# Performance work log

Hardware: AMD Instinct MI355X
Metric: run time of the kernel (lower is better)

Reference implementation:

```python
import jax, jax.numpy as jnp
import numpy as np

EPS_MSG = 1e-7
EPS_BN = 1e-5


def _seg_softmax(logits, seg, num_segments):
    # logits: [E, D] per-edge logits; softmax over edges sharing the same dst node
    m = jax.ops.segment_max(logits, seg, num_segments=num_segments)
    m = jnp.where(jnp.isfinite(m), m, 0.0)
    e = jnp.exp(logits - m[seg])
    s = jax.ops.segment_sum(e, seg, num_segments=num_segments)
    return e / (s[seg] + 1e-16)


def _batchnorm(h, gamma, beta):
    mu = jnp.mean(h, axis=0)
    var = jnp.var(h, axis=0)
    return (h - mu) * jax.lax.rsqrt(var + EPS_BN) * gamma + beta


def setup_inputs() -> dict:
    key = jax.random.key(0)
    ks = jax.random.split(key, 12)
    N, E, G, D, L = 100000, 600000, 512, 128, 7
    x = jax.random.randint(ks[0], (N, 9), 0, 64, dtype=jnp.int32)
    edge_index = jax.random.randint(ks[1], (2, E), 0, N, dtype=jnp.int32)
    edge_attr = jax.random.randint(ks[2], (E, 3), 0, 8, dtype=jnp.int32)
    batch = jnp.sort(jax.random.randint(ks[3], (N,), 0, G, dtype=jnp.int32))
    rf_pred = jax.random.uniform(ks[4], (G,), dtype=jnp.float32)
    atom_emb = jax.random.normal(ks[5], (9, 64, D), dtype=jnp.float32) * 0.02
    bond_emb = jax.random.normal(ks[6], (3, 8, D), dtype=jnp.float32) * 0.02
    conv_w = jax.random.normal(ks[7], (L, D, D), dtype=jnp.float32) * 0.02
    conv_b = jnp.zeros((L, D), dtype=jnp.float32)
    ts = jnp.ones((L,), dtype=jnp.float32)  # learnable inverse temperatures (init 1/t style)
    gammas = jnp.ones((L, D), dtype=jnp.float32)
    bn_betas = jnp.zeros((L, D), dtype=jnp.float32)
    final_w = jax.random.normal(ks[8], (D, 1), dtype=jnp.float32) * 0.02
    final_b = jnp.zeros((1,), dtype=jnp.float32)
    beta = jnp.array([0.5], dtype=jnp.float32)
    return {"x": x, "edge_index": edge_index, "edge_attr": edge_attr, "batch": batch,
            "rf_pred": rf_pred, "atom_emb": atom_emb, "bond_emb": bond_emb,
            "conv_w": conv_w, "conv_b": conv_b, "ts": ts, "gammas": gammas,
            "bn_betas": bn_betas, "final_w": final_w, "final_b": final_b, "beta": beta}


def reference(x, edge_index, edge_attr, batch, rf_pred, atom_emb, bond_emb,
              conv_w, conv_b, ts, gammas, bn_betas, final_w, final_b, beta):
    N = x.shape[0]
    G = rf_pred.shape[0]
    L = conv_w.shape[0]
    src, dst = edge_index[0], edge_index[1]

    # AtomEncoder / BondEncoder: sum of per-feature embeddings
    h = jax.vmap(lambda tab, idx: tab[idx], in_axes=(0, 1))(atom_emb, x).sum(0)          # [N, D]
    e_emb = jax.vmap(lambda tab, idx: tab[idx], in_axes=(0, 1))(bond_emb, edge_attr).sum(0)  # [E, D]

    def genconv(l, hin):
        msg = jax.nn.relu(hin[src] + e_emb) + EPS_MSG          # [E, D]
        alpha = _seg_softmax(msg * ts[l], dst, N)              # softmax aggregation weights
        aggr = jax.ops.segment_sum(alpha * msg, dst, num_segments=N)  # [N, D]
        return (hin + aggr) @ conv_w[l] + conv_b[l]

    # res+ DeeperGCN
    h = genconv(0, h)
    for l in range(1, L):
        h2 = jax.nn.relu(_batchnorm(h, gammas[l - 1], bn_betas[l - 1]))
        h = genconv(l, h2) + h
    h = jax.nn.relu(_batchnorm(h, gammas[L - 1], bn_betas[L - 1]))

    # mean graph pooling
    counts = jnp.maximum(jax.ops.segment_sum(jnp.ones((N,), h.dtype), batch, num_segments=G), 1.0)
    hg = jax.ops.segment_sum(h, batch, num_segments=G) / counts[:, None]  # [G, D]

    dgcn_pred = hg @ final_w + final_b  # [G, 1]
    return (1.0 - beta) * jax.nn.sigmoid(dgcn_pred) + beta * rf_pred.reshape(-1, 1)
```

## Files before the change

### kernel.cpp

```cpp
#include <hip/hip_runtime.h>
#include <hip/hip_fp16.h>
#include <math.h>

#define D 128
#define PF 12

typedef _Float16 f16x8 __attribute__((ext_vector_type(8)));
typedef float f32x4_t __attribute__((ext_vector_type(4)));


__global__ void hist_kernel(const int* __restrict__ edge_index, int* __restrict__ deg, int E) {
    int e = blockIdx.x * blockDim.x + threadIdx.x;
    if (e >= E) return;
    atomicAdd(&deg[edge_index[E + e]], 1);
}

__global__ void scanA_kernel(const int* __restrict__ deg, int* __restrict__ bsum, int n) {
    __shared__ int red[256];
    int b = blockIdx.x, t = threadIdx.x;
    int base = b * 1024 + t * 4;
    int s = 0;
#pragma unroll
    for (int j = 0; j < 4; ++j)
        if (base + j < n) s += deg[base + j];
    red[t] = s;
    __syncthreads();
    for (int off = 128; off > 0; off >>= 1) {
        if (t < off) red[t] += red[t + off];
        __syncthreads();
    }
    if (t == 0) bsum[b] = red[0];
}

__global__ void scanB_kernel(int* __restrict__ bsum, int nb) {
    __shared__ int sh[256];
    int t = threadIdx.x;
    sh[t] = (t < nb) ? bsum[t] : 0;
    __syncthreads();
    for (int off = 1; off < 256; off <<= 1) {
        int v = (t >= off) ? sh[t - off] : 0;
        __syncthreads();
        sh[t] += v;
        __syncthreads();
    }
    if (t < nb) bsum[t] = (t == 0) ? 0 : sh[t - 1];
}

__global__ void scanC_kernel(const int* __restrict__ deg, const int* __restrict__ boff,
                             int* __restrict__ row_start, int* __restrict__ cursor, int n) {
    __shared__ int sh[256];
    int b = blockIdx.x, t = threadIdx.x;
    int base = b * 1024 + t * 4;
    int v[4];
#pragma unroll
    for (int j = 0; j < 4; ++j) v[j] = (base + j < n) ? deg[base + j] : 0;
    int p[4];
    p[0] = 0; p[1] = v[0]; p[2] = v[0] + v[1]; p[3] = v[0] + v[1] + v[2];
    int s = p[3] + v[3];
    sh[t] = s;
    __syncthreads();
    for (int off = 1; off < 256; off <<= 1) {
        int x = (t >= off) ? sh[t - off] : 0;
        __syncthreads();
        sh[t] += x;
        __syncthreads();
    }
    int off0 = boff[b] + sh[t] - s;
#pragma unroll
    for (int j = 0; j < 4; ++j)
        if (base + j < n) {
            row_start[base + j] = off0 + p[j];
            cursor[base + j] = off0 + p[j];
        }
    if (base <= n - 1 && n - 1 < base + 4) row_start[n] = off0 + s;
}

__global__ void scatter_kernel(const int* __restrict__ edge_index, const int* __restrict__ edge_attr,
                               int* __restrict__ cursor, int2* __restrict__ csr, int E) {
    int e = blockIdx.x * blockDim.x + threadIdx.x;
    if (e >= E) return;
    int src = edge_index[e];
    int dst = edge_index[E + e];
    int pos = atomicAdd(&cursor[dst], 1);
    int a0 = edge_attr[e * 3], a1 = edge_attr[e * 3 + 1], a2 = edge_attr[e * 3 + 2];
    csr[pos] = make_int2(src, a0 | (a1 << 3) | (a2 << 6));
}

__global__ void misc_build_kernel(const float* __restrict__ bond_emb, __half2* __restrict__ evt,
                                  const float* __restrict__ conv_w, _Float16* __restrict__ wt,
                                  int wtTotal, const int* __restrict__ batch,
                                  int* __restrict__ gstart, int N, int G) {
    int idx = blockIdx.x * blockDim.x + threadIdx.x;
    if (idx < 512 * 64) {
        int combo = idx >> 6, j = idx & 63;
        int d0 = 2 * j;
        float ex = bond_emb[(combo & 7) * D + d0] +
                   bond_emb[(8 + ((combo >> 3) & 7)) * D + d0] +
                   bond_emb[(16 + ((combo >> 6) & 7)) * D + d0];
        float ey = bond_emb[(combo & 7) * D + d0 + 1] +
                   bond_emb[(8 + ((combo >> 3) & 7)) * D + d0 + 1] +
                   bond_emb[(16 + ((combo >> 6) & 7)) * D + d0 + 1];
        evt[idx] = __floats2half2_rn(ex, ey);
        return;
    }
    int widx = idx - 512 * 64;
    if (widx < wtTotal) {
        int l = widx >> 14;
        int rem = widx & 16383;
        int n = rem >> 7, k = rem & 127;
        wt[widx] = (_Float16)conv_w[(l << 14) + k * 128 + n];
        return;
    }
    int n = widx - wtTotal;
    if (n >= N) return;
    if (n == 0) {
        for (int g = 0; g <= batch[0]; ++g) gstart[g] = 0;
    } else {
        int b0 = batch[n - 1], b1 = batch[n];
        for (int g = b0 + 1; g <= b1; ++g) gstart[g] = n;
    }
    if (n == N - 1) {
        for (int g = batch[N - 1] + 1; g <= G; ++g) gstart[g] = N;
    }
}


__global__ void atom_embed_kernel(const int* __restrict__ x,
                                  const float* __restrict__ atom_emb,
                                  _Float16* __restrict__ h16, int N) {
    long long idx = (long long)blockIdx.x * blockDim.x + threadIdx.x;
    if (idx >= (long long)N * D) return;
    int n = (int)(idx >> 7);
    int d = (int)(idx & 127);
    float acc = 0.f;
#pragma unroll
    for (int f = 0; f < 9; ++f) {
        int v = x[n * 9 + f];
        acc += atom_emb[(long long)(f * 64 + v) * D + d];
    }
    h16[idx] = (_Float16)acc;
}

__global__ void bn_reduce_finalize_kernel(const float* __restrict__ partial, int nb,
                                          const float* __restrict__ gamma,
                                          const float* __restrict__ bnbeta, float invN,
                                          float* __restrict__ aArr, float* __restrict__ bArr) {
    __shared__ float r1[256], r2[256];
    int d = blockIdx.x, t = threadIdx.x;
    float a1 = 0.f, a2 = 0.f;
    for (int i = t; i < nb; i += 256) {
        a1 += partial[(long long)i * 256 + d];
        a2 += partial[(long long)i * 256 + 128 + d];
    }
    r1[t] = a1; r2[t] = a2;
    __syncthreads();
    for (int off = 128; off > 0; off >>= 1) {
        if (t < off) { r1[t] += r1[t + off]; r2[t] += r2[t + off]; }
        __syncthreads();
    }
    if (t == 0) {
        float mean = r1[0] * invN;
        float var = r2[0] * invN - mean * mean;
        float a = rsqrtf(var + 1e-5f) * gamma[d];
        aArr[d] = a;
        bArr[d] = bnbeta[d] - mean * a;
    }
}

__global__ __launch_bounds__(128, 8) void fused_layer_kernel(
        const __half2* __restrict__ h16c,
        const float* __restrict__ aArr, const float* __restrict__ bArr, int applyBN,
        const float* __restrict__ ts, int l,
        const int* __restrict__ row_start, const int2* __restrict__ csr,
        const __half2* __restrict__ evt,
        const _Float16* __restrict__ wt, const float* __restrict__ bias,
        int residual, _Float16* __restrict__ h16out,
        float* __restrict__ partial, int N) {
    __shared__ __align__(16) char smem[8192];
    _Float16* yh = (_Float16*)smem;
    __half2* tile = (__half2*)smem;

    int t = threadIdx.x;
    int row0 = blockIdx.x * 16;
    int wave = t >> 6;
    int lane = t & 63;
    float tsl = ts[l];
    int a = row0 + wave * 8;

    float2 bnA = make_float2(1.f, 0.f), bnB = make_float2(0.f, 0.f);
    if (applyBN) {
        bnA = ((const float2*)aArr)[lane];
        bnB = ((const float2*)bArr)[lane];
    }

    int rsv = row_start[min(a + min(lane, 8), N)];
    __half2 zero2 = __floats2half2_rn(0.f, 0.f);
    __half2 hsv0 = zero2, hsv1 = zero2, hsv2 = zero2, hsv3 = zero2;
    __half2 hsv4 = zero2, hsv5 = zero2, hsv6 = zero2, hsv7 = zero2;
    if (a + 0 < N) hsv0 = h16c[(size_t)(a + 0) * 64 + lane];
    if (a + 1 < N) hsv1 = h16c[(size_t)(a + 1) * 64 + lane];
    if (a + 2 < N) hsv2 = h16c[(size_t)(a + 2) * 64 + lane];
    if (a + 3 < N) hsv3 = h16c[(size_t)(a + 3) * 64 + lane];
    if (a + 4 < N) hsv4 = h16c[(size_t)(a + 4) * 64 + lane];
    if (a + 5 < N) hsv5 = h16c[(size_t)(a + 5) * 64 + lane];
    if (a + 6 < N) hsv6 = h16c[(size_t)(a + 6) * 64 + lane];
    if (a + 7 < N) hsv7 = h16c[(size_t)(a + 7) * 64 + lane];

    int s0 = __builtin_amdgcn_readlane(rsv, 0);
    int s1 = __builtin_amdgcn_readlane(rsv, 8);

    int c0 = s0;
    int2 eaCur = make_int2(0, 0), eaNxt = make_int2(0, 0);
    if (c0 + lane < s1) eaCur = csr[c0 + lane];
    if (c0 + 64 + lane < s1) eaNxt = csr[c0 + 64 + lane];

    __half2 hvS[PF], evS[PF];
#pragma unroll
    for (int k = 0; k < PF; ++k) {
        int pp = s0 + k;
        if (pp < s1) {
            int srcp = __builtin_amdgcn_readlane(eaCur.x, k);
            int cbp = __builtin_amdgcn_readlane(eaCur.y, k);
            hvS[k] = h16c[(size_t)srcp * 64 + lane];
            evS[k] = evt[(size_t)cbp * 64 + lane];
        }
    }

    float accwx = 0.f, accwy = 0.f, accmx = 0.f, accmy = 0.f;
    int cur = 0;
    int nend = __builtin_amdgcn_readlane(rsv, 1);

#define CLOSE_ROW()                                                          \
    {                                                                        \
        __half2 hh;                                                          \
        switch (cur) {                                                       \
            case 0: hh = hsv0; break;                                        \
            case 1: hh = hsv1; break;                                        \
            case 2: hh = hsv2; break;                                        \
            case 3: hh = hsv3; break;                                        \
            case 4: hh = hsv4; break;                                        \
            case 5: hh = hsv5; break;                                        \
            case 6: hh = hsv6; break;                                        \
            default: hh = hsv7; break;                                       \
        }                                                                    \
        float2 hs2 = __half22float2(hh);                                     \
        if (applyBN) {                                                       \
            hs2.x = fmaxf(hs2.x * bnA.x + bnB.x, 0.f);                       \
            hs2.y = fmaxf(hs2.y * bnA.y + bnB.y, 0.f);                       \
        }                                                                    \
        float2 yy;                                                           \
        yy.x = hs2.x + accmx / (accwx + 1e-16f);                             \
        yy.y = hs2.y + accmy / (accwy + 1e-16f);                             \
        tile[(wave * 8 + cur) * 68 + lane] = __floats2half2_rn(yy.x, yy.y);  \
        accwx = accwy = accmx = accmy = 0.f;                                 \
        cur++;                                                               \
        nend = __builtin_amdgcn_readlane(rsv, min(cur + 1, 8));              \
    }

    while (cur < 8 && nend == s0) CLOSE_ROW();

    int total = s1 - s0;
    for (int it = 0; it < total; it += PF) {
#pragma unroll
        for (int k = 0; k < PF; ++k) {
            int p = s0 + it + k;
            if (p < s1) {
                float2 hv = __half22float2(hvS[k]);
                float2 ev = __half22float2(evS[k]);
                if (applyBN) {
                    hv.x = fmaxf(hv.x * bnA.x + bnB.x, 0.f);
                    hv.y = fmaxf(hv.y * bnA.y + bnB.y, 0.f);
                }
                float mx = fmaxf(hv.x + ev.x, 0.f) + 1e-7f;
                float my = fmaxf(hv.y + ev.y, 0.f) + 1e-7f;
                float wx = __expf(mx * tsl);
                float wy = __expf(my * tsl);
                accwx += wx; accmx += wx * mx;
                accwy += wy; accmy += wy * my;
                int pp = p + PF;
                if (pp < s1) {
                    if (pp >= c0 + 64) {
                        c0 += 64;
                        eaCur = eaNxt;
                        eaNxt = make_int2(0, 0);
                        if (c0 + 64 + lane < s1) eaNxt = csr[c0 + 64 + lane];
                    }
                    int q = pp - c0;
                    int srcp = __builtin_amdgcn_readlane(eaCur.x, q);
                    int cbp = __builtin_amdgcn_readlane(eaCur.y, q);
                    hvS[k] = h16c[(size_t)srcp * 64 + lane];
                    evS[k] = evt[(size_t)cbp * 64 + lane];
                }
                while (cur < 8 && nend == p + 1) CLOSE_ROW();
            }
        }
    }
#undef CLOSE_ROW
    __syncthreads();

    int ln = t & 15;
    int quad = (t & 63) >> 4;
    const _Float16* h16in = (const _Float16*)h16c;

    float cs[4] = {0.f, 0.f, 0.f, 0.f};
    float cq[4] = {0.f, 0.f, 0.f, 0.f};
    const _Float16* ap = yh + ln * 136 + quad * 8;
#pragma unroll
    for (int ct = 0; ct < 4; ++ct) {
        int colg = (wave * 4 + ct) * 16 + ln;
        const _Float16* bp = wt + (size_t)colg * 128 + quad * 8;
        f32x4_t c = {0.f, 0.f, 0.f, 0.f};
#pragma unroll
        for (int kk = 0; kk < 4; ++kk) {
            f16x8 av = *(const f16x8*)(ap + kk * 32);
            f16x8 bv = *(const f16x8*)(bp + kk * 32);
            c = __builtin_amdgcn_mfma_f32_16x16x32_f16(av, bv, c, 0, 0, 0);
        }
        float bsv = bias[colg];
#pragma unroll
        for (int reg = 0; reg < 4; ++reg) {
            int r = row0 + quad * 4 + reg;
            if (r < N) {
                long long off = (long long)r * D + colg;
                float o = c[reg] + bsv;
                if (residual) o += (float)h16in[off];
                h16out[off] = (_Float16)o;
                cs[ct] += o; cq[ct] += o * o;
            }
        }
    }

    __syncthreads();
    float* stats = (float*)smem;
    int grp = wave * 4 + quad;
#pragma unroll
    for (int ct = 0; ct < 4; ++ct) {
        int colg = (wave * 4 + ct) * 16 + ln;
        stats[grp * 256 + colg] = cs[ct];
        stats[grp * 256 + 128 + colg] = cq[ct];
    }
    __syncthreads();
    float ssumA = 0.f, ssumB = 0.f;
#pragma unroll
    for (int g = 0; g < 8; ++g) {
        ssumA += stats[g * 256 + t];
        ssumB += stats[g * 256 + 128 + t];
    }
    partial[(long long)blockIdx.x * 256 + t] = ssumA;
    partial[(long long)blockIdx.x * 256 + 128 + t] = ssumB;
}

__global__ void pool_head_kernel(const _Float16* __restrict__ h16, const float* __restrict__ aArr,
                                 const float* __restrict__ bArr, const int* __restrict__ gstart,
                                 const float* __restrict__ fw, const float* __restrict__ fb,
                                 const float* __restrict__ beta, const float* __restrict__ rf,
                                 float* __restrict__ out) {
    __shared__ float red[256];
    int g = blockIdx.x, t = threadIdx.x;
    int d = t & 127, half = t >> 7;
    int s0 = gstart[g], s1 = gstart[g + 1];
    float a = aArr[d], b = bArr[d];
    float acc = 0.f;
    for (int n = s0 + half; n < s1; n += 2)
        acc += fmaxf((float)h16[(long long)n * D + d] * a + b, 0.f);
    red[t] = acc;
    __syncthreads();
    if (t < 128) red[t] += red[t + 128];
    __syncthreads();
    if (t < 64) {
        float v = red[t] * fw[t] + red[t + 64] * fw[t + 64];
#pragma unroll
        for (int off = 32; off > 0; off >>= 1) v += __shfl_down(v, off);
        if (t == 0) {
            float c = fmaxf((float)(s1 - s0), 1.f);
            float pred = v / c + fb[0];
            float sig = 1.f / (1.f + __expf(-pred));
            float bb = beta[0];
            out[g] = (1.f - bb) * sig + bb * rf[g];
        }
    }
}

static inline size_t align16(size_t x) { return (x + 15) & ~(size_t)15; }

extern "C" void kernel_launch(void* const* d_in, const int* in_sizes, int n_in,
                              void* d_out, int out_size, void* d_ws, size_t ws_size,
                              hipStream_t stream) {
    const int* x = (const int*)d_in[0];
    const int* edge_index = (const int*)d_in[1];
    const int* edge_attr = (const int*)d_in[2];
    const int* batch = (const int*)d_in[3];
    const float* rf_pred = (const float*)d_in[4];
    const float* atom_emb = (const float*)d_in[5];
    const float* bond_emb = (const float*)d_in[6];
    const float* conv_w = (const float*)d_in[7];
    const float* conv_b = (const float*)d_in[8];
    const float* ts = (const float*)d_in[9];
    const float* gammas = (const float*)d_in[10];
    const float* bn_betas = (const float*)d_in[11];
    const float* final_w = (const float*)d_in[12];
    const float* final_b = (const float*)d_in[13];
    const float* beta = (const float*)d_in[14];
    float* out = (float*)d_out;

    int N = in_sizes[0] / 9;
    int E = in_sizes[1] / 2;
    int G = in_sizes[4];
    int L = in_sizes[9];

    int nTiles = (N + 15) / 16;
    size_t ND = (size_t)N * D;

    char* p = (char*)d_ws;
    _Float16* h16_a = (_Float16*)p;  p += align16(ND * 2);
    _Float16* h16_b = (_Float16*)p;  p += align16(ND * 2);
    __half2* evt = (__half2*)p;      p += align16((size_t)512 * 64 * 4);
    _Float16* wt = (_Float16*)p;     p += align16((size_t)L * 16384 * 2);
    float* partial = (float*)p;      p += align16((size_t)256 * nTiles * 4);
    float* aArr = (float*)p;         p += align16((size_t)D * 4);
    float* bArr = (float*)p;         p += align16((size_t)D * 4);
    int* gstart = (int*)p;           p += align16((size_t)(G + 1) * 4);
    int* deg = (int*)p;              p += align16((size_t)N * 4);
    int* row_start = (int*)p;        p += align16((size_t)(N + 1) * 4);
    int* cursor = (int*)p;           p += align16((size_t)N * 4);
    int* bsum = (int*)p;             p += align16((size_t)256 * 4);
    int2* csr = (int2*)p;            p += align16((size_t)E * 8);

    long long ndThreads = (long long)N * D;
    int ndBlocks = (int)((ndThreads + 255) / 256);
    int eBlocks = (E + 255) / 256;
    int nb1024 = (N + 1023) / 1024;
    int wtTotal = L * 16384;
    int miscTotal = 512 * 64 + wtTotal + N;
    int miscBlocks = (miscTotal + 255) / 256;
    float invN = 1.0f / (float)N;

    hipMemsetAsync(deg, 0, (size_t)N * sizeof(int), stream);
    hist_kernel<<<eBlocks, 256, 0, stream>>>(edge_index, deg, E);
    scanA_kernel<<<nb1024, 256, 0, stream>>>(deg, bsum, N);
    scanB_kernel<<<1, 256, 0, stream>>>(bsum, nb1024);
    scanC_kernel<<<nb1024, 256, 0, stream>>>(deg, bsum, row_start, cursor, N);
    scatter_kernel<<<eBlocks, 256, 0, stream>>>(edge_index, edge_attr, cursor, csr, E);
    misc_build_kernel<<<miscBlocks, 256, 0, stream>>>(bond_emb, evt, conv_w, wt, wtTotal,
                                                      batch, gstart, N, G);

    atom_embed_kernel<<<ndBlocks, 256, 0, stream>>>(x, atom_emb, h16_a, N);

    _Float16* h16c = h16_a;
    _Float16* h16n = h16_b;
    for (int l = 0; l < L; ++l) {
        int applyBN = (l >= 1) ? 1 : 0;
        if (applyBN) {
            bn_reduce_finalize_kernel<<<128, 256, 0, stream>>>(
                partial, nTiles, gammas + (size_t)(l - 1) * D,
                bn_betas + (size_t)(l - 1) * D, invN, aArr, bArr);
        }
        fused_layer_kernel<<<nTiles, 128, 0, stream>>>(
            (const __half2*)h16c, aArr, bArr, applyBN, ts, l, row_start, csr, evt,
            wt + (size_t)l * 16384, conv_b + (size_t)l * D,
            applyBN, h16n, partial, N);
        _Float16* tmp16 = h16c; h16c = h16n; h16n = tmp16;
    }

    bn_reduce_finalize_kernel<<<128, 256, 0, stream>>>(
        partial, nTiles, gammas + (size_t)(L - 1) * D,
        bn_betas + (size_t)(L - 1) * D, invN, aArr, bArr);
    pool_head_kernel<<<G, 256, 0, stream>>>(h16c, aArr, bArr, gstart,
                                            final_w, final_b, beta, rf_pred, out);
}
```

Measured before the change: 880.5 us.

## Make each wave own a full 16-row tile and drop block syncs

Each wave now handles a whole 16-row tile: it does the gather/softmax aggregation for 16 rows and then all 8 MFMA column tiles, and two tiles are packed per block. This removes both __syncthreads and the shared-memory stats reduction, which is replaced by wave shuffles writing per-tile partials. It also moves the BN and message relu math to packed fp16 and lowers the prefetch depth from 12 to 8. In exchange each wave holds more registers (16 hsv, 8 accumulator sets) and some arithmetic now runs at fp16 precision.

```diff
diff --git a/kernel.cpp b/kernel.cpp
--- a/kernel.cpp
+++ b/kernel.cpp
@@ -3,10 +3,18 @@
 #include <math.h>
 
 #define D 128
-#define PF 12
+#define PF 8
 
 typedef _Float16 f16x8 __attribute__((ext_vector_type(8)));
+typedef _Float16 f16x2 __attribute__((ext_vector_type(2)));
 typedef float f32x4_t __attribute__((ext_vector_type(4)));
+
+static __device__ __forceinline__ f16x2 h2v(__half2 h) {
+    union { __half2 h; f16x2 v; } u; u.h = h; return u.v;
+}
+static __device__ __forceinline__ __half2 v2h(f16x2 v) {
+    union { f16x2 v; __half2 h; } u; u.v = v; return u.h;
+}
 
 
 __global__ void hist_kernel(const int* __restrict__ edge_index, int* __restrict__ deg, int E) {
@@ -175,39 +183,54 @@
         const __half2* __restrict__ evt,
         const _Float16* __restrict__ wt, const float* __restrict__ bias,
         int residual, _Float16* __restrict__ h16out,
-        float* __restrict__ partial, int N) {
-    __shared__ __align__(16) char smem[8192];
+        float* __restrict__ partial, int nTiles, int N) {
+    __shared__ __align__(16) char smem[8704];
     _Float16* yh = (_Float16*)smem;
-    __half2* tile = (__half2*)smem;
+    __half2* tile2 = (__half2*)smem;
 
     int t = threadIdx.x;
-    int row0 = blockIdx.x * 16;
     int wave = t >> 6;
     int lane = t & 63;
+    int tile = blockIdx.x * 2 + wave;
+    if (tile >= nTiles) return;
+    int row0 = tile * 16;
     float tsl = ts[l];
-    int a = row0 + wave * 8;
-
-    float2 bnA = make_float2(1.f, 0.f), bnB = make_float2(0.f, 0.f);
+
+    f16x2 zerov = (f16x2)(_Float16)0;
+    f16x2 bnA2 = zerov, bnB2 = zerov;
     if (applyBN) {
-        bnA = ((const float2*)aArr)[lane];
-        bnB = ((const float2*)bArr)[lane];
-    }
-
-    int rsv = row_start[min(a + min(lane, 8), N)];
-    __half2 zero2 = __floats2half2_rn(0.f, 0.f);
+        float2 af = ((const float2*)aArr)[lane];
+        float2 bf = ((const float2*)bArr)[lane];
+        bnA2[0] = (_Float16)af.x; bnA2[1] = (_Float16)af.y;
+        bnB2[0] = (_Float16)bf.x; bnB2[1] = (_Float16)bf.y;
+    }
+
+    int rsv = row_start[min(row0 + min(lane, 16), N)];
+
+    __half2 zero2 = v2h(zerov);
     __half2 hsv0 = zero2, hsv1 = zero2, hsv2 = zero2, hsv3 = zero2;
     __half2 hsv4 = zero2, hsv5 = zero2, hsv6 = zero2, hsv7 = zero2;
-    if (a + 0 < N) hsv0 = h16c[(size_t)(a + 0) * 64 + lane];
-    if (a + 1 < N) hsv1 = h16c[(size_t)(a + 1) * 64 + lane];
-    if (a + 2 < N) hsv2 = h16c[(size_t)(a + 2) * 64 + lane];
-    if (a + 3 < N) hsv3 = h16c[(size_t)(a + 3) * 64 + lane];
-    if (a + 4 < N) hsv4 = h16c[(size_t)(a + 4) * 64 + lane];
-    if (a + 5 < N) hsv5 = h16c[(size_t)(a + 5) * 64 + lane];
-    if (a + 6 < N) hsv6 = h16c[(size_t)(a + 6) * 64 + lane];
-    if (a + 7 < N) hsv7 = h16c[(size_t)(a + 7) * 64 + lane];
+    __half2 hsv8 = zero2, hsv9 = zero2, hsv10 = zero2, hsv11 = zero2;
+    __half2 hsv12 = zero2, hsv13 = zero2, hsv14 = zero2, hsv15 = zero2;
+    if (row0 + 0 < N) hsv0 = h16c[(size_t)(row0 + 0) * 64 + lane];
+    if (row0 + 1 < N) hsv1 = h16c[(size_t)(row0 + 1) * 64 + lane];
+    if (row0 + 2 < N) hsv2 = h16c[(size_t)(row0 + 2) * 64 + lane];
+    if (row0 + 3 < N) hsv3 = h16c[(size_t)(row0 + 3) * 64 + lane];
+    if (row0 + 4 < N) hsv4 = h16c[(size_t)(row0 + 4) * 64 + lane];
+    if (row0 + 5 < N) hsv5 = h16c[(size_t)(row0 + 5) * 64 + lane];
+    if (row0 + 6 < N) hsv6 = h16c[(size_t)(row0 + 6) * 64 + lane];
+    if (row0 + 7 < N) hsv7 = h16c[(size_t)(row0 + 7) * 64 + lane];
+    if (row0 + 8 < N) hsv8 = h16c[(size_t)(row0 + 8) * 64 + lane];
+    if (row0 + 9 < N) hsv9 = h16c[(size_t)(row0 + 9) * 64 + lane];
+    if (row0 + 10 < N) hsv10 = h16c[(size_t)(row0 + 10) * 64 + lane];
+    if (row0 + 11 < N) hsv11 = h16c[(size_t)(row0 + 11) * 64 + lane];
+    if (row0 + 12 < N) hsv12 = h16c[(size_t)(row0 + 12) * 64 + lane];
+    if (row0 + 13 < N) hsv13 = h16c[(size_t)(row0 + 13) * 64 + lane];
+    if (row0 + 14 < N) hsv14 = h16c[(size_t)(row0 + 14) * 64 + lane];
+    if (row0 + 15 < N) hsv15 = h16c[(size_t)(row0 + 15) * 64 + lane];
 
     int s0 = __builtin_amdgcn_readlane(rsv, 0);
-    int s1 = __builtin_amdgcn_readlane(rsv, 8);
+    int s1 = __builtin_amdgcn_readlane(rsv, 16);
 
     int c0 = s0;
     int2 eaCur = make_int2(0, 0), eaNxt = make_int2(0, 0);
@@ -230,34 +253,32 @@
     int cur = 0;
     int nend = __builtin_amdgcn_readlane(rsv, 1);
 
-#define CLOSE_ROW()                                                          \
-    {                                                                        \
-        __half2 hh;                                                          \
-        switch (cur) {                                                       \
-            case 0: hh = hsv0; break;                                        \
-            case 1: hh = hsv1; break;                                        \
-            case 2: hh = hsv2; break;                                        \
-            case 3: hh = hsv3; break;                                        \
-            case 4: hh = hsv4; break;                                        \
-            case 5: hh = hsv5; break;                                        \
-            case 6: hh = hsv6; break;                                        \
-            default: hh = hsv7; break;                                       \
-        }                                                                    \
-        float2 hs2 = __half22float2(hh);                                     \
-        if (applyBN) {                                                       \
-            hs2.x = fmaxf(hs2.x * bnA.x + bnB.x, 0.f);                       \
-            hs2.y = fmaxf(hs2.y * bnA.y + bnB.y, 0.f);                       \
-        }                                                                    \
-        float2 yy;                                                           \
-        yy.x = hs2.x + accmx / (accwx + 1e-16f);                             \
-        yy.y = hs2.y + accmy / (accwy + 1e-16f);                             \
-        tile[(wave * 8 + cur) * 68 + lane] = __floats2half2_rn(yy.x, yy.y);  \
-        accwx = accwy = accmx = accmy = 0.f;                                 \
-        cur++;                                                               \
-        nend = __builtin_amdgcn_readlane(rsv, min(cur + 1, 8));              \
-    }
-
-    while (cur < 8 && nend == s0) CLOSE_ROW();
+#define CLOSE_ROW()                                                           \
+    {                                                                         \
+        __half2 hh;                                                           \
+        switch (cur) {                                                        \
+            case 0: hh = hsv0; break;   case 1: hh = hsv1; break;             \
+            case 2: hh = hsv2; break;   case 3: hh = hsv3; break;             \
+            case 4: hh = hsv4; break;   case 5: hh = hsv5; break;             \
+            case 6: hh = hsv6; break;   case 7: hh = hsv7; break;             \
+            case 8: hh = hsv8; break;   case 9: hh = hsv9; break;             \
+            case 10: hh = hsv10; break; case 11: hh = hsv11; break;           \
+            case 12: hh = hsv12; break; case 13: hh = hsv13; break;           \
+            case 14: hh = hsv14; break; default: hh = hsv15; break;           \
+        }                                                                     \
+        f16x2 hvv = h2v(hh);                                                  \
+        if (applyBN)                                                          \
+            hvv = __builtin_elementwise_max(hvv * bnA2 + bnB2, zerov);        \
+        float2 yy;                                                            \
+        yy.x = (float)hvv[0] + accmx / (accwx + 1e-16f);                      \
+        yy.y = (float)hvv[1] + accmy / (accwy + 1e-16f);                      \
+        tile2[(wave * 16 + cur) * 68 + lane] = __floats2half2_rn(yy.x, yy.y); \
+        accwx = accwy = accmx = accmy = 0.f;                                  \
+        cur++;                                                                \
+        nend = __builtin_amdgcn_readlane(rsv, min(cur + 1, 16));              \
+    }
+
+    while (cur < 16 && nend == s0) CLOSE_ROW();
 
     int total = s1 - s0;
     for (int it = 0; it < total; it += PF) {
@@ -265,18 +286,16 @@
         for (int k = 0; k < PF; ++k) {
             int p = s0 + it + k;
             if (p < s1) {
-                float2 hv = __half22float2(hvS[k]);
-                float2 ev = __half22float2(evS[k]);
-                if (applyBN) {
-                    hv.x = fmaxf(hv.x * bnA.x + bnB.x, 0.f);
-                    hv.y = fmaxf(hv.y * bnA.y + bnB.y, 0.f);
-                }
-                float mx = fmaxf(hv.x + ev.x, 0.f) + 1e-7f;
-                float my = fmaxf(hv.y + ev.y, 0.f) + 1e-7f;
+                f16x2 hv2 = h2v(hvS[k]);
+                if (applyBN)
+                    hv2 = __builtin_elementwise_max(hv2 * bnA2 + bnB2, zerov);
+                f16x2 m2 = __builtin_elementwise_max(hv2 + h2v(evS[k]), zerov);
+                float mx = (float)m2[0] + 1e-7f;
+                float my = (float)m2[1] + 1e-7f;
                 float wx = __expf(mx * tsl);
                 float wy = __expf(my * tsl);
-                accwx += wx; accmx += wx * mx;
-                accwy += wy; accmy += wy * my;
+                accwx += wx; accmx = fmaf(wx, mx, accmx);
+                accwy += wy; accmy = fmaf(wy, my, accmy);
                 int pp = p + PF;
                 if (pp < s1) {
                     if (pp >= c0 + 64) {
@@ -291,23 +310,21 @@
                     hvS[k] = h16c[(size_t)srcp * 64 + lane];
                     evS[k] = evt[(size_t)cbp * 64 + lane];
                 }
-                while (cur < 8 && nend == p + 1) CLOSE_ROW();
+                while (cur < 16 && nend == p + 1) CLOSE_ROW();
             }
         }
     }
 #undef CLOSE_ROW
-    __syncthreads();
-
-    int ln = t & 15;
-    int quad = (t & 63) >> 4;
+
+    int ln = lane & 15;
+    int quad = lane >> 4;
     const _Float16* h16in = (const _Float16*)h16c;
-
-    float cs[4] = {0.f, 0.f, 0.f, 0.f};
-    float cq[4] = {0.f, 0.f, 0.f, 0.f};
-    const _Float16* ap = yh + ln * 136 + quad * 8;
-#pragma unroll
-    for (int ct = 0; ct < 4; ++ct) {
-        int colg = (wave * 4 + ct) * 16 + ln;
+    const _Float16* ap = yh + (wave * 16 + ln) * 136 + quad * 8;
+
+    float csv[8], cqv[8];
+#pragma unroll
+    for (int ct = 0; ct < 8; ++ct) {
+        int colg = ct * 16 + ln;
         const _Float16* bp = wt + (size_t)colg * 128 + quad * 8;
         f32x4_t c = {0.f, 0.f, 0.f, 0.f};
 #pragma unroll
@@ -317,6 +334,7 @@
             c = __builtin_amdgcn_mfma_f32_16x16x32_f16(av, bv, c, 0, 0, 0);
         }
         float bsv = bias[colg];
+        float cs = 0.f, cq = 0.f;
 #pragma unroll
         for (int reg = 0; reg < 4; ++reg) {
             int r = row0 + quad * 4 + reg;
@@ -325,29 +343,25 @@
                 float o = c[reg] + bsv;
                 if (residual) o += (float)h16in[off];
                 h16out[off] = (_Float16)o;
-                cs[ct] += o; cq[ct] += o * o;
+                cs += o; cq += o * o;
             }
         }
-    }
-
-    __syncthreads();
-    float* stats = (float*)smem;
-    int grp = wave * 4 + quad;
-#pragma unroll
-    for (int ct = 0; ct < 4; ++ct) {
-        int colg = (wave * 4 + ct) * 16 + ln;
-        stats[grp * 256 + colg] = cs[ct];
-        stats[grp * 256 + 128 + colg] = cq[ct];
-    }
-    __syncthreads();
-    float ssumA = 0.f, ssumB = 0.f;
-#pragma unroll
-    for (int g = 0; g < 8; ++g) {
-        ssumA += stats[g * 256 + t];
-        ssumB += stats[g * 256 + 128 + t];
-    }
-    partial[(long long)blockIdx.x * 256 + t] = ssumA;
-    partial[(long long)blockIdx.x * 256 + 128 + t] = ssumB;
+        csv[ct] = cs; cqv[ct] = cq;
+    }
+
+#pragma unroll
+    for (int ct = 0; ct < 8; ++ct) {
+        float s = csv[ct];
+        s += __shfl_xor(s, 16);
+        s += __shfl_xor(s, 32);
+        float q = cqv[ct];
+        q += __shfl_xor(q, 16);
+        q += __shfl_xor(q, 32);
+        if (quad == 0) {
+            partial[(long long)tile * 256 + ct * 16 + ln] = s;
+            partial[(long long)tile * 256 + 128 + ct * 16 + ln] = q;
+        }
+    }
 }
 
 __global__ void pool_head_kernel(const _Float16* __restrict__ h16, const float* __restrict__ aArr,
@@ -433,9 +447,10 @@
     int wtTotal = L * 16384;
     int miscTotal = 512 * 64 + wtTotal + N;
     int miscBlocks = (miscTotal + 255) / 256;
+    int fusedBlocks = (nTiles + 1) / 2;
     float invN = 1.0f / (float)N;
 
-    hipMemsetAsync(deg, 0, (size_t)N * sizeof(int), stream);
+    (void)hipMemsetAsync(deg, 0, (size_t)N * sizeof(int), stream);
     hist_kernel<<<eBlocks, 256, 0, stream>>>(edge_index, deg, E);
     scanA_kernel<<<nb1024, 256, 0, stream>>>(deg, bsum, N);
     scanB_kernel<<<1, 256, 0, stream>>>(bsum, nb1024);
@@ -455,10 +470,10 @@
                 partial, nTiles, gammas + (size_t)(l - 1) * D,
                 bn_betas + (size_t)(l - 1) * D, invN, aArr, bArr);
         }
-        fused_layer_kernel<<<nTiles, 128, 0, stream>>>(
+        fused_layer_kernel<<<fusedBlocks, 128, 0, stream>>>(
             (const __half2*)h16c, aArr, bArr, applyBN, ts, l, row_start, csr, evt,
             wt + (size_t)l * 16384, conv_b + (size_t)l * D,
-            applyBN, h16n, partial, N);
+            applyBN, h16n, partial, nTiles, N);
         _Float16* tmp16 = h16c; h16c = h16n; h16n = tmp16;
     }
 
```

Measured after the change: 934.2 us. 1.06x slower.
